# Kernel tuning notes

Hardware: AMD Instinct MI355X
Metric: run time of the kernel (lower is better)

Reference implementation:

```python
import jax, jax.numpy as jnp
import numpy as np

ND, NZ = 8192, 4096        # drug / disease node counts
IN, HID = 256, 128         # in_dim / hidden_dim
MID = (IN + HID) // 2      # projector mid width = 192
P = 4                      # metapaths per node type
M = P + 1                  # +1 raw-feature channel
DEG = 32                   # avg degree of each metapath adjacency


def _spmm_agg(feat, att, src, dst, n):
    # feat (n,IN); att (M,n,1) (only first P rows used, like the torch zip); src,dst (P,E)
    def one(a, s, d):
        deg = jax.ops.segment_sum(jnp.ones(s.shape, jnp.float32), s, num_segments=n)
        inv = 1.0 / jnp.maximum(deg, 1.0)          # L1 row-normalized adjacency values
        x = a * feat                               # node-feature attention gating (n,IN)
        return jax.ops.segment_sum(inv[s][:, None] * x[d], s, num_segments=n)
    agg = jax.vmap(one)(att[:P], src, dst)         # (P,n,IN)
    return jnp.concatenate([feat[None], agg], axis=0)   # (M,n,IN): raw feat + metapath aggs


def _projector(x, W1, b1, W2, b2, W3, b3):
    # per-metapath 3-layer MLP (dropout is eval-mode identity)
    h = jax.nn.relu(jnp.einsum('mni,mio->mno', x, W1) + b1[:, None, :])
    h = jax.nn.relu(jnp.einsum('mni,mio->mno', h, W2) + b2[:, None, :])
    return jnp.einsum('mni,mio->mno', h, W3) + b3[:, None, :]   # (M,n,HID)


def _metapath_attn(proj, Wq, bq, Wk, bk, beta):
    # per-node attention over the M metapath channels; V is computed but unused in the original
    p = jnp.transpose(proj, (1, 0, 2))             # (n,M,HID)
    q = p @ Wq + bq
    k = p @ Wk + bk
    attn = jax.nn.softmax(jnp.einsum('nmh,nkh->nmk', q, k), axis=-1)
    out = beta * jnp.einsum('nmk,nkh->nmh', attn, p) + p        # (n,M,HID)
    return out.reshape(M, p.shape[0], HID)         # faithful torch .view (NOT a transpose)


def reference(feat_drug, feat_disease, att_drug, att_disease,
              drug_src, drug_dst, disease_src, disease_dst,
              dW1, db1, dW2, db2, dW3, db3,
              zW1, zb1, zW2, zb2, zW3, zb3,
              Wq_d, bq_d, Wk_d, bk_d, beta_d,
              Wq_z, bq_z, Wk_z, bk_z, beta_z,
              weight_attn, Wdec, bdec):
    aggr_d = _spmm_agg(feat_drug, att_drug, drug_src, drug_dst, ND)
    aggr_z = _spmm_agg(feat_disease, att_disease, disease_src, disease_dst, NZ)
    proj_d = _projector(aggr_d, dW1, db1, dW2, db2, dW3, db3)          # (M,ND,HID)
    proj_z = _projector(aggr_z, zW1, zb1, zW2, zb2, zW3, zb3)          # (M,NZ,HID)
    out_d = _metapath_attn(proj_d, Wq_d, bq_d, Wk_d, bk_d, beta_d)     # (M,ND,HID)
    out_z = _metapath_attn(proj_z, Wq_z, bq_z, Wk_z, bk_z, beta_z)     # (M,NZ,HID)
    # Multiplex inner-product decoder
    dec_z = jnp.einsum('mzh,mhk->mzk', out_z, Wdec) + bdec[:, None, :]
    preds = jnp.einsum('mdh,mzh->mdz', out_d, dec_z)                   # (M,ND,NZ)
    w = jax.nn.softmax(weight_attn, axis=0)                            # (M,1,1)
    return jnp.sum(preds * w, axis=0)                                  # (ND,NZ)


def setup_inputs() -> dict:
    key = jax.random.key(0)
    ks = iter(jax.random.split(key, 48))
    f32 = jnp.float32
    def nrm(shape, scale=0.05):
        return jax.random.normal(next(ks), shape, f32) * scale
    inp = {}
    inp['feat_drug'] = nrm((ND, IN), 1.0)
    inp['feat_disease'] = nrm((NZ, IN), 1.0)
    inp['att_drug'] = jax.random.uniform(next(ks), (M, ND, 1), f32)
    inp['att_disease'] = jax.random.uniform(next(ks), (M, NZ, 1), f32)
    inp['drug_src'] = jax.random.randint(next(ks), (P, ND * DEG), 0, ND, jnp.int32)
    inp['drug_dst'] = jax.random.randint(next(ks), (P, ND * DEG), 0, ND, jnp.int32)
    inp['disease_src'] = jax.random.randint(next(ks), (P, NZ * DEG), 0, NZ, jnp.int32)
    inp['disease_dst'] = jax.random.randint(next(ks), (P, NZ * DEG), 0, NZ, jnp.int32)
    for t in ('d', 'z'):
        inp[t + 'W1'] = nrm((M, IN, MID));  inp[t + 'b1'] = jnp.zeros((M, MID), f32)
        inp[t + 'W2'] = nrm((M, MID, MID)); inp[t + 'b2'] = jnp.zeros((M, MID), f32)
        inp[t + 'W3'] = nrm((M, MID, HID)); inp[t + 'b3'] = jnp.zeros((M, HID), f32)
        inp['Wq_' + t] = nrm((HID, HID));   inp['bq_' + t] = jnp.zeros((HID,), f32)
        inp['Wk_' + t] = nrm((HID, HID));   inp['bk_' + t] = jnp.zeros((HID,), f32)
        inp['beta_' + t] = jnp.ones((1,), f32)
    inp['weight_attn'] = nrm((M, 1, 1), 1.0)
    inp['Wdec'] = nrm((M, HID, HID))
    inp['bdec'] = jnp.zeros((M, HID), f32)
    return inp
```

## Files before the change

kernel.cpp:

```cpp
#include <hip/hip_runtime.h>
#include <hip/hip_bf16.h>

#define ND 8192
#define NZ 4096
#define IN_DIM 256
#define HID 128
#define MIDW 192
#define NP 4
#define NCH 5
#define DEG 32
#define E_D (ND*DEG)
#define E_Z (NZ*DEG)
#define CAP 96

typedef __hip_bfloat16 bf16;
typedef __attribute__((ext_vector_type(8))) short s8v;
typedef __attribute__((ext_vector_type(4))) float f4v;

static __device__ __forceinline__ unsigned short f2bf(float x){
  bf16 b = __float2bfloat16(x);
  return *reinterpret_cast<unsigned short*>(&b);
}
static __device__ __forceinline__ uint packbf2(float a, float b){
  return (uint)f2bf(a) | ((uint)f2bf(b) << 16);
}
static __device__ __forceinline__ float bfl(uint w){ return __uint_as_float(w<<16); }
static __device__ __forceinline__ float bfh(uint w){ return __uint_as_float(w & 0xffff0000u); }
static __device__ __forceinline__ void gload16(const void* g, void* l){
  __builtin_amdgcn_global_load_lds(
      (const __attribute__((address_space(1))) unsigned int*)g,
      (__attribute__((address_space(3))) unsigned int*)l, 16, 0, 0);
}

static __device__ __forceinline__ void tpz(const float* __restrict__ in, bf16* __restrict__ out,
                                           int rows, int cols, long idx){
  int per = rows*cols;
  int b = (int)(idx / per);
  int rem = (int)(idx - (long)b*per);
  int r = rem / cols, c = rem - r*cols;
  out[(long)b*per + (long)c*rows + r] = __float2bfloat16(in[idx]);
}

#define B_SD 0
#define B_SZ 4096
#define B_CD 6144
#define B_CZ 8192
#define B_W1D 9216
#define B_W1Z 10176
#define B_W2D 11136
#define B_W2Z 11856
#define B_W3D 12576
#define B_W3Z 13056
#define B_WDEC 13536
#define B_G 13856
#define B_V 13984
#define B_END 13985

__global__ __launch_bounds__(256) void k_prep(
    const int* __restrict__ src_d, const int* __restrict__ dst_d,
    const int* __restrict__ src_z, const int* __restrict__ dst_z,
    int* __restrict__ cur_d, int* __restrict__ cur_z,
    int* __restrict__ edl_d, int* __restrict__ edl_z,
    const float* feat_d, const float* feat_z, bf16* featb_d, bf16* featb_z,
    const float* dW1, const float* dW2, const float* dW3,
    const float* zW1, const float* zW2, const float* zW3,
    bf16* w1t_d, bf16* w2t_d, bf16* w3t_d, bf16* w1t_z, bf16* w2t_z, bf16* w3t_z,
    const float* Wdec, bf16* wdect,
    const float* Wq_d, const float* Wk_d, const float* Wq_z, const float* Wk_z,
    bf16* Gtb,
    const float* bq_d, const float* bq_z, float* v2v,
    const float* wattn, float* wsm)
{
  int b = blockIdx.x, t = threadIdx.x;
  if (b < B_SZ){
    long i = (long)b*256 + t;
    int m = (int)(i >> 18);
    int s = src_d[i];
    int pos = atomicAdd(&cur_d[(m<<13) + s], 1);
    if (pos < CAP) edl_d[((long)((m<<13) + s))*CAP + pos] = dst_d[i];
  } else if (b < B_CD){
    long j = (long)(b - B_SZ)*256 + t;
    int m = (int)(j >> 17);
    int s = src_z[j];
    int pos = atomicAdd(&cur_z[(m<<12) + s], 1);
    if (pos < CAP) edl_z[((long)((m<<12) + s))*CAP + pos] = dst_z[j];
  } else if (b < B_CZ){
    long i4 = (long)(b - B_CD)*256 + t;
    float4 v = ((const float4*)feat_d)[i4];
    ushort4 o; o.x=f2bf(v.x); o.y=f2bf(v.y); o.z=f2bf(v.z); o.w=f2bf(v.w);
    ((ushort4*)featb_d)[i4] = o;
  } else if (b < B_W1D){
    long i4 = (long)(b - B_CZ)*256 + t;
    float4 v = ((const float4*)feat_z)[i4];
    ushort4 o; o.x=f2bf(v.x); o.y=f2bf(v.y); o.z=f2bf(v.z); o.w=f2bf(v.w);
    ((ushort4*)featb_z)[i4] = o;
  } else if (b < B_W1Z){ tpz(dW1, w1t_d, IN_DIM, MIDW, (long)(b-B_W1D)*256 + t); }
  else if (b < B_W2D){ tpz(zW1, w1t_z, IN_DIM, MIDW, (long)(b-B_W1Z)*256 + t); }
  else if (b < B_W2Z){ tpz(dW2, w2t_d, MIDW, MIDW, (long)(b-B_W2D)*256 + t); }
  else if (b < B_W3D){ tpz(zW2, w2t_z, MIDW, MIDW, (long)(b-B_W2Z)*256 + t); }
  else if (b < B_W3Z){ tpz(dW3, w3t_d, MIDW, HID, (long)(b-B_W3D)*256 + t); }
  else if (b < B_WDEC){ tpz(zW3, w3t_z, MIDW, HID, (long)(b-B_W3Z)*256 + t); }
  else if (b < B_G){ tpz(Wdec, wdect, HID, HID, (long)(b-B_WDEC)*256 + t); }
  else if (b < B_V){
    int cc = (b - B_G)*2 + (t>>7);
    int hp = t & 127;
    const float* Wq = cc < 128 ? Wq_d : Wq_z;
    const float* Wk = cc < 128 ? Wk_d : Wk_z;
    int c = cc & 127;
    float s = 0.f;
    for (int j=0;j<HID;j++) s += Wq[hp*HID+j]*Wk[c*HID+j];
    Gtb[(cc < 128 ? 0 : HID*HID) + c*HID + hp] = __float2bfloat16(s);
  } else {
    if (t < 128){
      float s = 0.f;
      for (int j=0;j<HID;j++) s += Wk_d[t*HID+j]*bq_d[j];
      v2v[t] = s;
    } else {
      int tt = t-128;
      float s = 0.f;
      for (int j=0;j<HID;j++) s += Wk_z[tt*HID+j]*bq_z[j];
      v2v[128+tt] = s;
    }
    if (t == 0){
      float mx = wattn[0];
      for (int i=1;i<NCH;i++) mx = fmaxf(mx, wattn[i]);
      float e[NCH], s=0.f;
      for (int i=0;i<NCH;i++){ e[i]=expf(wattn[i]-mx); s+=e[i]; }
      for (int i=0;i<NCH;i++) wsm[i]=e[i]/s;
    }
  }
}

__global__ __launch_bounds__(256) void k_stage1(
    const bf16* __restrict__ featb_d, const bf16* __restrict__ featb_z,
    const bf16* __restrict__ w1t_d, const bf16* __restrict__ w1t_z,
    const float* __restrict__ db1, const float* __restrict__ zb1,
    const float* __restrict__ att_d, const float* __restrict__ att_z,
    bf16* __restrict__ h1_d, bf16* __restrict__ h1_z,
    bf16* __restrict__ Y_d, bf16* __restrict__ Y_z)
{
  int z = blockIdx.z, typ = z/5, c = z - 5*(z/5);
  int n = typ ? NZ : ND;
  long row0 = (long)blockIdx.x*128;
  if (row0 >= n) return;
  int col0 = blockIdx.y*64;
  __shared__ short As[128*40];
  __shared__ short Bs[64*40];
  int t = threadIdx.x, lane = t&63, wv = t>>6;
  int l15 = lane&15, kof = (lane>>4)*8;
  const short* Ag = (const short*)(typ ? featb_z : featb_d);
  const short* Bg = (const short*)(typ ? w1t_z : w1t_d) + (long)c*MIDW*IN_DIM;
  f4v acc[2][4] = {};
  for (int kk=0; kk<IN_DIM; kk+=32){
    __syncthreads();
    #pragma unroll
    for (int j=0;j<2;j++){
      int c2 = t + j*256;
      int row = c2>>2, sub = c2&3;
      *(s8v*)(&As[row*40 + sub*8]) = *(const s8v*)(Ag + (row0+row)*IN_DIM + kk + sub*8);
    }
    { int row = t>>2, sub = t&3;
      *(s8v*)(&Bs[row*40 + sub*8]) = *(const s8v*)(Bg + (long)(col0+row)*IN_DIM + kk + sub*8); }
    __syncthreads();
    s8v af[2], bfr[4];
    #pragma unroll
    for (int i2=0;i2<2;i2++) af[i2] = *(const s8v*)(&As[(wv*32 + i2*16 + l15)*40 + kof]);
    #pragma unroll
    for (int j2=0;j2<4;j2++) bfr[j2] = *(const s8v*)(&Bs[(j2*16 + l15)*40 + kof]);
    #pragma unroll
    for (int i2=0;i2<2;i2++)
      #pragma unroll
      for (int j2=0;j2<4;j2++)
        acc[i2][j2] = __builtin_amdgcn_mfma_f32_16x16x32_bf16(af[i2], bfr[j2], acc[i2][j2],0,0,0);
  }
  if (c == 0){
    const float* bb = typ ? zb1 : db1;
    bf16* outp = typ ? h1_z : h1_d;
    #pragma unroll
    for (int i2=0;i2<2;i2++)
      #pragma unroll
      for (int j2=0;j2<4;j2++){
        int col = col0 + j2*16 + l15;
        float bv = bb[col];
        #pragma unroll
        for (int r=0;r<4;r++){
          long row = row0 + wv*32 + i2*16 + (lane>>4)*4 + r;
          outp[row*MIDW + col] = __float2bfloat16(fmaxf(acc[i2][j2][r] + bv, 0.f));
        }
      }
  } else {
    const float* rs = (typ ? att_z : att_d) + (long)(c-1)*n;
    bf16* outp = (typ ? Y_z : Y_d) + (long)(c-1)*n*MIDW;
    #pragma unroll
    for (int i2=0;i2<2;i2++)
      #pragma unroll
      for (int j2=0;j2<4;j2++){
        int col = col0 + j2*16 + l15;
        #pragma unroll
        for (int r=0;r<4;r++){
          long row = row0 + wv*32 + i2*16 + (lane>>4)*4 + r;
          outp[row*MIDW + col] = __float2bfloat16(acc[i2][j2][r] * rs[row]);
        }
      }
  }
}

__global__ __launch_bounds__(256) void k_agg2(
    const int* __restrict__ edl_d, const int* __restrict__ cur_d, const float* __restrict__ bias_d,
    const bf16* __restrict__ Y_d, bf16* __restrict__ h1_d,
    const int* __restrict__ edl_z, const int* __restrict__ cur_z, const float* __restrict__ bias_z,
    const bf16* __restrict__ Y_z, bf16* __restrict__ h1_z)
{
  int wid = (blockIdx.x*256 + threadIdx.x) >> 6;
  int lane = threadIdx.x & 63;
  const int *edl, *cur; const float* bias; const uint* Yb; bf16* h1; int n, m;
  if (wid < NP*ND){
    m = wid >> 13; int s0 = wid & (ND-1);
    edl = edl_d; cur = cur_d; bias = bias_d; h1 = h1_d; n = ND;
    Yb = (const uint*)Y_d + (long)m*ND*96;
    wid = s0;
  } else {
    int w2 = wid - NP*ND;
    m = w2 >> 12; int s0 = w2 & (NZ-1);
    edl = edl_z; cur = cur_z; bias = bias_z; h1 = h1_z; n = NZ;
    Yb = (const uint*)Y_z + (long)m*NZ*96;
    wid = s0;
  }
  int s = wid;
  int cnt0 = cur[(long)m*n + s];
  int cnt = cnt0 < CAP ? cnt0 : CAP;
  const int* lp = edl + ((long)m*n + s)*CAP;
  bool hi2 = lane < 32;
  float a0=0.f,a1=0.f,a2=0.f,a3=0.f;
  for (int base=0; base<cnt; base+=64){
    int rem = cnt - base;
    int idx = (lane < rem) ? lane : (rem-1);
    int e = lp[base + idx];
    int lim = rem < 64 ? rem : 64;
    int j = 0;
    for (; j+1<lim; j+=2){
      int d0 = __shfl(e, j), d1 = __shfl(e, j+1);
      const uint* r0 = Yb + (long)d0*96;
      const uint* r1 = Yb + (long)d1*96;
      uint w0 = r0[lane], w1 = r1[lane];
      uint v0 = hi2 ? r0[64+lane] : 0u;
      uint v1 = hi2 ? r1[64+lane] : 0u;
      a0 += bfl(w0)+bfl(w1); a1 += bfh(w0)+bfh(w1);
      a2 += bfl(v0)+bfl(v1); a3 += bfh(v0)+bfh(v1);
    }
    if (j < lim){
      int d0 = __shfl(e, j);
      const uint* r0 = Yb + (long)d0*96;
      uint w0 = r0[lane];
      uint v0 = hi2 ? r0[64+lane] : 0u;
      a0 += bfl(w0); a1 += bfh(w0);
      a2 += bfl(v0); a3 += bfh(v0);
    }
  }
  float inv = 1.0f / fmaxf((float)cnt0, 1.0f);
  const float* bb = bias + (m+1)*MIDW;
  float2 b0 = *(const float2*)(bb + 2*lane);
  uint* hrow = (uint*)((short*)h1 + ((long)(m+1)*n + s)*MIDW);
  hrow[lane] = packbf2(fmaxf(a0*inv + b0.x, 0.f), fmaxf(a1*inv + b0.y, 0.f));
  if (hi2){
    float2 b1v = *(const float2*)(bb + 128 + 2*lane);
    hrow[64+lane] = packbf2(fmaxf(a2*inv + b1v.x, 0.f), fmaxf(a3*inv + b1v.y, 0.f));
  }
}

struct GemmP {
  const bf16* A; const bf16* BT; const float* bias; bf16* out;
  const float* scale; const float* rowsc;
  long rs_moff, a_moff, out_rstride, out_moff;
  int K, N, nrows, relu;
};

__global__ __launch_bounds__(256) void k_gemm(GemmP P0, GemmP P1, int zsplit)
{
  const GemmP& p = ((int)blockIdx.z < zsplit) ? P0 : P1;
  int m = ((int)blockIdx.z < zsplit) ? blockIdx.z : blockIdx.z - zsplit;
  long row0 = (long)blockIdx.x*128;
  if (row0 >= p.nrows) return;
  int col0 = blockIdx.y*64;
  if (col0 >= p.N) return;
  __shared__ short As[128*40];
  __shared__ short Bs[64*40];
  int t = threadIdx.x;
  const short* Ag = (const short*)p.A + m*p.a_moff;
  const short* Bg = (const short*)p.BT + (long)m*p.N*p.K;
  int lane = t&63, wv = t>>6;
  int l15 = lane&15, kof = (lane>>4)*8;
  int K = p.K;
  f4v acc[2][4] = {};
  for (int kk=0; kk<K; kk+=32){
    __syncthreads();
    #pragma unroll
    for (int j=0;j<2;j++){
      int c = t + j*256;
      int row = c>>2, sub = c&3;
      *(s8v*)(&As[row*40 + sub*8]) = *(const s8v*)(Ag + (row0+row)*K + kk + sub*8);
    }
    { int row = t>>2, sub = t&3;
      *(s8v*)(&Bs[row*40 + sub*8]) = *(const s8v*)(Bg + (long)(col0+row)*K + kk + sub*8); }
    __syncthreads();
    s8v af[2], bfr[4];
    #pragma unroll
    for (int i2=0;i2<2;i2++) af[i2] = *(const s8v*)(&As[(wv*32 + i2*16 + l15)*40 + kof]);
    #pragma unroll
    for (int j2=0;j2<4;j2++) bfr[j2] = *(const s8v*)(&Bs[(j2*16 + l15)*40 + kof]);
    #pragma unroll
    for (int i2=0;i2<2;i2++)
      #pragma unroll
      for (int j2=0;j2<4;j2++)
        acc[i2][j2] = __builtin_amdgcn_mfma_f32_16x16x32_bf16(af[i2], bfr[j2], acc[i2][j2],0,0,0);
  }
  float sc = p.scale ? p.scale[m] : 1.0f;
  #pragma unroll
  for (int i2=0;i2<2;i2++){
    #pragma unroll
    for (int j2=0;j2<4;j2++){
      int col = col0 + j2*16 + l15;
      float bv = p.bias ? p.bias[m*p.N + col] : 0.f;
      #pragma unroll
      for (int r=0;r<4;r++){
        long row = row0 + wv*32 + i2*16 + (lane>>4)*4 + r;
        float v = acc[i2][j2][r] + bv;
        if (p.relu) v = fmaxf(v, 0.f);
        v *= sc;
        if (p.rowsc) v *= p.rowsc[m*p.rs_moff + row];
        p.out[m*p.out_moff + row*p.out_rstride + col] = __float2bfloat16(v);
      }
    }
  }
}

struct MlpP { const bf16* h1; const bf16* w2t; const float* b2;
              const bf16* w3t; const float* b3; bf16* pout; bf16* pgout;
              const bf16* gt; int n; };

__global__ __launch_bounds__(256) void k_mlp23(MlpP P0, MlpP P1, int zsplit)
{
  const MlpP& p = ((int)blockIdx.z < zsplit) ? P0 : P1;
  int m = ((int)blockIdx.z < zsplit) ? blockIdx.z : blockIdx.z - zsplit;
  int row0 = blockIdx.x*128;
  if (row0 >= p.n) return;
  __shared__ short h2s[128*200];
  __shared__ short As[128*40];
  __shared__ short Bs[192*40];
  int t = threadIdx.x, lane = t&63, wv = t>>6;
  int l15 = lane&15, hi = lane>>4, kof = hi*8;
  const short* Ag = (const short*)p.h1 + ((long)m*p.n + row0)*MIDW;
  const short* Bg = (const short*)p.w2t + (long)m*MIDW*MIDW;
  f4v accA[2][12] = {};
  for (int kk=0; kk<MIDW; kk+=32){
    __syncthreads();
    #pragma unroll
    for (int j=0;j<2;j++){
      int c = t + j*256;
      int row = c>>2, sub = c&3;
      *(s8v*)(&As[row*40 + sub*8]) = *(const s8v*)(Ag + (long)row*MIDW + kk + sub*8);
    }
    #pragma unroll
    for (int j=0;j<3;j++){
      int c = t + j*256;
      int row = c>>2, sub = c&3;
      *(s8v*)(&Bs[row*40 + sub*8]) = *(const s8v*)(Bg + (long)row*MIDW + kk + sub*8);
    }
    __syncthreads();
    s8v af[2], bfr[12];
    #pragma unroll
    for (int i2=0;i2<2;i2++) af[i2] = *(const s8v*)(&As[(wv*32 + i2*16 + l15)*40 + kof]);
    #pragma unroll
    for (int j2=0;j2<12;j2++) bfr[j2] = *(const s8v*)(&Bs[(j2*16 + l15)*40 + kof]);
    #pragma unroll
    for (int i2=0;i2<2;i2++)
      #pragma unroll
      for (int j2=0;j2<12;j2++)
        accA[i2][j2] = __builtin_amdgcn_mfma_f32_16x16x32_bf16(af[i2], bfr[j2], accA[i2][j2],0,0,0);
  }
  float b2l[12];
  #pragma unroll
  for (int j2=0;j2<12;j2++) b2l[j2] = p.b2[m*MIDW + j2*16 + l15];
  #pragma unroll
  for (int i2=0;i2<2;i2++)
    #pragma unroll
    for (int j2=0;j2<12;j2++)
      #pragma unroll
      for (int r=0;r<4;r++){
        int rl = wv*32 + i2*16 + hi*4 + r;
        h2s[rl*200 + j2*16 + l15] = (short)f2bf(fmaxf(accA[i2][j2][r] + b2l[j2], 0.f));
      }
  const short* Cg = (const short*)p.w3t + (long)m*HID*MIDW;
  f4v accB[2][8] = {};
  for (int kk=0; kk<MIDW; kk+=32){
    __syncthreads();
    #pragma unroll
    for (int j=0;j<2;j++){
      int c = t + j*256;
      int row = c>>2, sub = c&3;
      *(s8v*)(&Bs[row*40 + sub*8]) = *(const s8v*)(Cg + (long)row*MIDW + kk + sub*8);
    }
    __syncthreads();
    s8v af[2], bfr[8];
    #pragma unroll
    for (int i2=0;i2<2;i2++) af[i2] = *(const s8v*)(&h2s[(wv*32 + i2*16 + l15)*200 + kk + kof]);
    #pragma unroll
    for (int j2=0;j2<8;j2++) bfr[j2] = *(const s8v*)(&Bs[(j2*16 + l15)*40 + kof]);
    #pragma unroll
    for (int i2=0;i2<2;i2++)
      #pragma unroll
      for (int j2=0;j2<8;j2++)
        accB[i2][j2] = __builtin_amdgcn_mfma_f32_16x16x32_bf16(af[i2], bfr[j2], accB[i2][j2],0,0,0);
  }
  __syncthreads();
  #pragma unroll
  for (int j2=0;j2<8;j2++){
    float b3v = p.b3[m*HID + j2*16 + l15];
    #pragma unroll
    for (int i2=0;i2<2;i2++)
      #pragma unroll
      for (int r=0;r<4;r++){
        int rl = wv*32 + i2*16 + hi*4 + r;
        unsigned short hv = f2bf(accB[i2][j2][r] + b3v);
        p.pout[((long)(row0+rl))*(NCH*HID) + m*HID + j2*16 + l15] = *(bf16*)&hv;
        h2s[rl*200 + j2*16 + l15] = (short)hv;
      }
  }
  const short* Gg = (const short*)p.gt;
  f4v accC[2][8] = {};
  for (int kk=0; kk<HID; kk+=32){
    __syncthreads();
    #pragma unroll
    for (int j=0;j<2;j++){
      int c = t + j*256;
      int row = c>>2, sub = c&3;
      *(s8v*)(&Bs[row*40 + sub*8]) = *(const s8v*)(Gg + (long)row*HID + kk + sub*8);
    }
    __syncthreads();
    s8v af[2], bfr[8];
    #pragma unroll
    for (int i2=0;i2<2;i2++) af[i2] = *(const s8v*)(&h2s[(wv*32 + i2*16 + l15)*200 + kk + kof]);
    #pragma unroll
    for (int j2=0;j2<8;j2++) bfr[j2] = *(const s8v*)(&Bs[(j2*16 + l15)*40 + kof]);
    #pragma unroll
    for (int i2=0;i2<2;i2++)
      #pragma unroll
      for (int j2=0;j2<8;j2++)
        accC[i2][j2] = __builtin_amdgcn_mfma_f32_16x16x32_bf16(af[i2], bfr[j2], accC[i2][j2],0,0,0);
  }
  #pragma unroll
  for (int j2=0;j2<8;j2++)
    #pragma unroll
    for (int i2=0;i2<2;i2++)
      #pragma unroll
      for (int r=0;r<4;r++){
        long row = row0 + wv*32 + i2*16 + hi*4 + r;
        p.pgout[row*(NCH*HID) + m*HID + j2*16 + l15] = __float2bfloat16(accC[i2][j2][r]);
      }
}

__global__ __launch_bounds__(64) void k_attn(
    const bf16* __restrict__ p_d, const bf16* __restrict__ pg_d, const float* __restrict__ v2v,
    const float* __restrict__ beta_d, bf16* __restrict__ o_d,
    const bf16* __restrict__ p_z, const bf16* __restrict__ pg_z,
    const float* __restrict__ beta_z, bf16* __restrict__ o_z)
{
  int node = blockIdx.x; int t = threadIdx.x;
  const bf16 *pp, *gg; bf16* outp; const float *betap, *v2p;
  if (node < ND){
    pp = p_d + (long)node*640; gg = pg_d + (long)node*640;
    outp = o_d + (long)node*640; betap = beta_d; v2p = v2v;
  } else {
    int nz = node - ND;
    pp = p_z + (long)nz*640; gg = pg_z + (long)nz*640;
    outp = o_z + (long)nz*640; betap = beta_z; v2p = v2v + 128;
  }
  __shared__ float pl[640], gl[640], v2l[128];
  __shared__ float lg[25], at[25], bv[5];
  const uint* pu = (const uint*)pp;
  const uint* gu = (const uint*)gg;
  for (int i=t; i<320; i+=64){
    uint w = pu[i];
    pl[2*i] = bfl(w); pl[2*i+1] = bfh(w);
    uint g = gu[i];
    gl[2*i] = bfl(g); gl[2*i+1] = bfh(g);
  }
  v2l[t] = v2p[t]; v2l[64+t] = v2p[64+t];
  __syncthreads();
  if (t < 60){
    int pr = t>>1, sub = t&1, h0 = sub*64;
    float s = 0.f;
    if (pr < 25){
      int mi = pr/5, ki = pr - 5*(pr/5);
      for (int h=h0; h<h0+64; h++) s += gl[mi*HID+h]*pl[ki*HID+h];
      s += __shfl_xor(s, 1);
      if (!sub) lg[pr] = s;
    } else {
      int k = pr - 25;
      for (int h=h0; h<h0+64; h++) s += pl[k*HID+h]*v2l[h];
      s += __shfl_xor(s, 1);
      if (!sub) bv[k] = s;
    }
  }
  __syncthreads();
  if (t < 5){
    float l0[5];
    for (int j=0;j<5;j++) l0[j] = lg[t*5+j] + bv[j];
    float mx = l0[0];
    for (int j=1;j<5;j++) mx = fmaxf(mx, l0[j]);
    float e[5], su=0.f;
    for (int j=0;j<5;j++){ e[j] = expf(l0[j]-mx); su += e[j]; }
    for (int j=0;j<5;j++) at[t*5+j] = e[j]/su;
  }
  __syncthreads();
  float bt = betap[0];
  for (int i=t; i<320; i+=64){
    int mm = i>>6, h = (i&63)*2;
    float s0=0.f, s1=0.f;
    #pragma unroll
    for (int k2=0;k2<5;k2++){
      s0 += at[mm*5+k2]*pl[k2*HID+h];
      s1 += at[mm*5+k2]*pl[k2*HID+h+1];
    }
    ((uint*)outp)[i] = packbf2(pl[2*i] + bt*s0, pl[2*i+1] + bt*s1);
  }
}

__global__ __launch_bounds__(256) void k_gemm_final(
    const bf16* __restrict__ Aout, const bf16* __restrict__ Bb, float* __restrict__ out)
{
  __shared__ short As[128*64];
  __shared__ short Bs[128*64];
  int t = threadIdx.x;
  int lane = t&63, wv=t>>6, wr=wv>>1, wc=wv&1;
  int row0 = blockIdx.x*128, col0 = blockIdx.y*128;
  const short* Ag = (const short*)Aout;
  const short* Bg = (const short*)Bb;
  int l15 = lane&15, hi = lane>>4;
  int srow = t>>3;
  int sseg = (t&7) ^ (srow&7);
  f4v acc[4][4] = {};
  for (int kk=0; kk<NCH*HID; kk+=64){
    int mch = kk>>7, h0 = kk&127;
    __syncthreads();
    #pragma unroll
    for (int j=0;j<4;j++){
      int row = j*32 + srow;
      gload16(Ag + ((long)mch*ND + row0+row)*HID + h0 + sseg*8,
              (char*)As + ((j*256 + t)<<4));
      gload16(Bg + (long)(col0+row)*(NCH*HID) + kk + sseg*8,
              (char*)Bs + ((j*256 + t)<<4));
    }
    asm volatile("s_waitcnt vmcnt(0)" ::: "memory");
    __syncthreads();
    #pragma unroll
    for (int sl=0; sl<2; sl++){
      s8v af[4], bg[4];
      #pragma unroll
      for (int i=0;i<4;i++){
        int ra = wr*64 + i*16 + l15;
        af[i] = *(const s8v*)(&As[ra*64 + (((sl*4+hi) ^ (ra&7))*8)]);
        int rb = wc*64 + i*16 + l15;
        bg[i] = *(const s8v*)(&Bs[rb*64 + (((sl*4+hi) ^ (rb&7))*8)]);
      }
      #pragma unroll
      for (int mi=0;mi<4;mi++)
        #pragma unroll
        for (int ni=0;ni<4;ni++)
          acc[mi][ni] = __builtin_amdgcn_mfma_f32_16x16x32_bf16(af[mi], bg[ni], acc[mi][ni],0,0,0);
    }
  }
  #pragma unroll
  for (int mi=0;mi<4;mi++){
    #pragma unroll
    for (int ni=0;ni<4;ni++){
      int col = col0 + wc*64 + ni*16 + l15;
      #pragma unroll
      for (int r=0;r<4;r++){
        int row = row0 + wr*64 + mi*16 + hi*4 + r;
        out[(long)row*NZ + col] = acc[mi][ni][r];
      }
    }
  }
}

extern "C" void kernel_launch(void* const* d_in, const int* in_sizes, int n_in,
                              void* d_out, int out_size, void* d_ws, size_t ws_size,
                              hipStream_t stream)
{
  (void)in_sizes; (void)n_in; (void)out_size;
  const float* feat_d = (const float*)d_in[0];
  const float* feat_z = (const float*)d_in[1];
  const float* att_d  = (const float*)d_in[2];
  const float* att_z  = (const float*)d_in[3];
  const int* src_d = (const int*)d_in[4];
  const int* dst_d = (const int*)d_in[5];
  const int* src_z = (const int*)d_in[6];
  const int* dst_z = (const int*)d_in[7];
  const float* dW1=(const float*)d_in[8];  const float* db1=(const float*)d_in[9];
  const float* dW2=(const float*)d_in[10]; const float* db2=(const float*)d_in[11];
  const float* dW3=(const float*)d_in[12]; const float* db3=(const float*)d_in[13];
  const float* Wq_d=(const float*)d_in[14]; const float* bq_d=(const float*)d_in[15];
  const float* Wk_d=(const float*)d_in[16]; const float* bk_d=(const float*)d_in[17];
  const float* beta_d=(const float*)d_in[18];
  const float* zW1=(const float*)d_in[19]; const float* zb1=(const float*)d_in[20];
  const float* zW2=(const float*)d_in[21]; const float* zb2=(const float*)d_in[22];
  const float* zW3=(const float*)d_in[23]; const float* zb3=(const float*)d_in[24];
  const float* Wq_z=(const float*)d_in[25]; const float* bq_z=(const float*)d_in[26];
  const float* Wk_z=(const float*)d_in[27]; const float* bk_z=(const float*)d_in[28];
  const float* beta_z=(const float*)d_in[29];
  const float* wattn=(const float*)d_in[30];
  const float* Wdec=(const float*)d_in[31]; const float* bdec=(const float*)d_in[32];
  (void)bk_d; (void)bk_z;

  char* ws = (char*)d_ws;
  size_t o = 0;
  auto alloc = [&](size_t bytes)->char*{
    size_t r = (o + 255) & ~(size_t)255;
    o = r + bytes;
    return ws + r;
  };
  bf16* featb_d = (bf16*)alloc((size_t)ND*IN_DIM*2);
  bf16* featb_z = (bf16*)alloc((size_t)NZ*IN_DIM*2);
  bf16* Y_d = (bf16*)alloc((size_t)NP*ND*MIDW*2);
  bf16* Y_z = (bf16*)alloc((size_t)NP*NZ*MIDW*2);
  bf16* h1_d = (bf16*)alloc((size_t)NCH*ND*MIDW*2);
  bf16* h1_z = (bf16*)alloc((size_t)NCH*NZ*MIDW*2);
  bf16* pbuf_d = (bf16*)alloc((size_t)ND*NCH*HID*2);
  int* edl_d = (int*)alloc((size_t)NP*ND*CAP*4);
  int* edl_z = (int*)alloc((size_t)NP*NZ*CAP*4);
  int* cur = (int*)alloc((size_t)(NP*ND + NP*NZ)*4);
  int* cur_d = cur;
  int* cur_z = cur + NP*ND;
  bf16* w1t_d = (bf16*)alloc((size_t)NCH*MIDW*IN_DIM*2);
  bf16* w2t_d = (bf16*)alloc((size_t)NCH*MIDW*MIDW*2);
  bf16* w3t_d = (bf16*)alloc((size_t)NCH*HID*MIDW*2);
  bf16* w1t_z = (bf16*)alloc((size_t)NCH*MIDW*IN_DIM*2);
  bf16* w2t_z = (bf16*)alloc((size_t)NCH*MIDW*MIDW*2);
  bf16* w3t_z = (bf16*)alloc((size_t)NCH*HID*MIDW*2);
  bf16* Gtb = (bf16*)alloc((size_t)2*HID*HID*2);
  bf16* wdect = (bf16*)alloc((size_t)NCH*HID*HID*2);
  float* v2v = (float*)alloc((size_t)256*4);
  float* wsm = (float*)alloc((size_t)NCH*4);
  bf16* out_d = h1_d;
  bf16* out_z = h1_z;
  bf16* pg_z  = Y_d;
  bf16* Bbig  = Y_z;
  bf16* pg_d  = (bf16*)edl_d;
  bf16* pbuf_z = (bf16*)edl_z;
  if (ws_size < o) return;

  hipMemsetAsync(cur, 0, (size_t)(NP*ND + NP*NZ)*4, stream);
  k_prep<<<B_END, 256, 0, stream>>>(src_d, dst_d, src_z, dst_z, cur_d, cur_z, edl_d, edl_z,
      feat_d, feat_z, featb_d, featb_z,
      dW1, dW2, dW3, zW1, zW2, zW3,
      w1t_d, w2t_d, w3t_d, w1t_z, w2t_z, w3t_z,
      Wdec, wdect, Wq_d, Wk_d, Wq_z, Wk_z, Gtb,
      bq_d, bq_z, v2v, wattn, wsm);
  k_stage1<<<dim3(64, 3, 10), 256, 0, stream>>>(featb_d, featb_z, w1t_d, w1t_z,
      db1, zb1, att_d, att_z, h1_d, h1_z, Y_d, Y_z);
  k_agg2<<<(NP*ND + NP*NZ)/4, 256, 0, stream>>>(edl_d, cur_d, db1, Y_d, h1_d,
                                                edl_z, cur_z, zb1, Y_z, h1_z);
  {
    MlpP pd = {h1_d, w2t_d, db2, w3t_d, db3, pbuf_d, pg_d, Gtb, ND};
    MlpP pz = {h1_z, w2t_z, zb2, w3t_z, zb3, pbuf_z, pg_z, Gtb + HID*HID, NZ};
    k_mlp23<<<dim3(64, 1, 10), 256, 0, stream>>>(pd, pz, 5);
  }
  k_attn<<<ND + NZ, 64, 0, stream>>>(pbuf_d, pg_d, v2v, beta_d, out_d,
                                     pbuf_z, pg_z, beta_z, out_z);
  {
    GemmP pz = {out_z, wdect, bdec, Bbig, wsm, nullptr, 0, (long)NZ*HID, (long)NCH*HID, HID, HID, HID, NZ, 0};
    k_gemm<<<dim3(32, 2, 5), 256, 0, stream>>>(pz, pz, 5);
  }
  k_gemm_final<<<dim3(64, 32), 256, 0, stream>>>(out_d, Bbig, (float*)d_out);
}
```

Measured before the change: 291.1 us.

## Move edge bucketing into stage-1 GEMM kernel and store neighbor lists as ushort

Edge bucketing (atomic counters plus neighbor-list writes) moves out of the prep kernel and into the front of the stage-1 GEMM kernel. Each of the 1920 blocks handles a slice of edges before its GEMM tile, so the scatter can overlap with matmul work from other blocks. Neighbor lists are stored as 16-bit indices, which halves their memory traffic in both the scatter and the aggregation gather. Workspace aliasing is reshuffled to fit the smaller buffers. Blocks that exit early for disease rows still do their edge share, and the extra atomics may delay the GEMM part of each block.

```diff
diff --git a/kernel.cpp b/kernel.cpp
--- a/kernel.cpp
+++ b/kernel.cpp
@@ -12,6 +12,8 @@
 #define E_D (ND*DEG)
 #define E_Z (NZ*DEG)
 #define CAP 96
+#define NEDGE (NP*E_D + NP*E_Z)
+#define EPB 820
 
 typedef __hip_bfloat16 bf16;
 typedef __attribute__((ext_vector_type(8))) short s8v;
@@ -41,26 +43,19 @@
   out[(long)b*per + (long)c*rows + r] = __float2bfloat16(in[idx]);
 }
 
-#define B_SD 0
-#define B_SZ 4096
-#define B_CD 6144
-#define B_CZ 8192
-#define B_W1D 9216
-#define B_W1Z 10176
-#define B_W2D 11136
-#define B_W2Z 11856
-#define B_W3D 12576
-#define B_W3Z 13056
-#define B_WDEC 13536
-#define B_G 13856
-#define B_V 13984
-#define B_END 13985
+#define B_CZ 2048
+#define B_W1D 3072
+#define B_W1Z 4032
+#define B_W2D 4992
+#define B_W2Z 5712
+#define B_W3D 6432
+#define B_W3Z 6912
+#define B_WDEC 7392
+#define B_G 7712
+#define B_V 7840
+#define B_END 7841
 
 __global__ __launch_bounds__(256) void k_prep(
-    const int* __restrict__ src_d, const int* __restrict__ dst_d,
-    const int* __restrict__ src_z, const int* __restrict__ dst_z,
-    int* __restrict__ cur_d, int* __restrict__ cur_z,
-    int* __restrict__ edl_d, int* __restrict__ edl_z,
     const float* feat_d, const float* feat_z, bf16* featb_d, bf16* featb_z,
     const float* dW1, const float* dW2, const float* dW3,
     const float* zW1, const float* zW2, const float* zW3,
@@ -72,20 +67,8 @@
     const float* wattn, float* wsm)
 {
   int b = blockIdx.x, t = threadIdx.x;
-  if (b < B_SZ){
-    long i = (long)b*256 + t;
-    int m = (int)(i >> 18);
-    int s = src_d[i];
-    int pos = atomicAdd(&cur_d[(m<<13) + s], 1);
-    if (pos < CAP) edl_d[((long)((m<<13) + s))*CAP + pos] = dst_d[i];
-  } else if (b < B_CD){
-    long j = (long)(b - B_SZ)*256 + t;
-    int m = (int)(j >> 17);
-    int s = src_z[j];
-    int pos = atomicAdd(&cur_z[(m<<12) + s], 1);
-    if (pos < CAP) edl_z[((long)((m<<12) + s))*CAP + pos] = dst_z[j];
-  } else if (b < B_CZ){
-    long i4 = (long)(b - B_CD)*256 + t;
+  if (b < B_CZ){
+    long i4 = (long)b*256 + t;
     float4 v = ((const float4*)feat_d)[i4];
     ushort4 o; o.x=f2bf(v.x); o.y=f2bf(v.y); o.z=f2bf(v.z); o.w=f2bf(v.w);
     ((ushort4*)featb_d)[i4] = o;
@@ -132,6 +115,10 @@
 }
 
 __global__ __launch_bounds__(256) void k_stage1(
+    const int* __restrict__ src_d, const int* __restrict__ dst_d,
+    const int* __restrict__ src_z, const int* __restrict__ dst_z,
+    int* __restrict__ cur_d, int* __restrict__ cur_z,
+    ushort* __restrict__ edl_d, ushort* __restrict__ edl_z,
     const bf16* __restrict__ featb_d, const bf16* __restrict__ featb_z,
     const bf16* __restrict__ w1t_d, const bf16* __restrict__ w1t_z,
     const float* __restrict__ db1, const float* __restrict__ zb1,
@@ -139,6 +126,24 @@
     bf16* __restrict__ h1_d, bf16* __restrict__ h1_z,
     bf16* __restrict__ Y_d, bf16* __restrict__ Y_z)
 {
+  int t = threadIdx.x;
+  {
+    int bid = blockIdx.x + 64*(blockIdx.y + 3*blockIdx.z);
+    int e0 = bid*EPB;
+    int e1 = e0 + EPB < NEDGE ? e0 + EPB : NEDGE;
+    for (int e = e0 + t; e < e1; e += 256){
+      if (e < NP*E_D){
+        int m = e>>18, s = src_d[e];
+        int pos = atomicAdd(&cur_d[(m<<13)+s], 1);
+        if (pos < CAP) edl_d[((long)((m<<13)+s))*CAP + pos] = (ushort)dst_d[e];
+      } else {
+        int j = e - NP*E_D;
+        int m = j>>17, s = src_z[j];
+        int pos = atomicAdd(&cur_z[(m<<12)+s], 1);
+        if (pos < CAP) edl_z[((long)((m<<12)+s))*CAP + pos] = (ushort)dst_z[j];
+      }
+    }
+  }
   int z = blockIdx.z, typ = z/5, c = z - 5*(z/5);
   int n = typ ? NZ : ND;
   long row0 = (long)blockIdx.x*128;
@@ -146,7 +151,7 @@
   int col0 = blockIdx.y*64;
   __shared__ short As[128*40];
   __shared__ short Bs[64*40];
-  int t = threadIdx.x, lane = t&63, wv = t>>6;
+  int lane = t&63, wv = t>>6;
   int l15 = lane&15, kof = (lane>>4)*8;
   const short* Ag = (const short*)(typ ? featb_z : featb_d);
   const short* Bg = (const short*)(typ ? w1t_z : w1t_d) + (long)c*MIDW*IN_DIM;
@@ -206,14 +211,14 @@
 }
 
 __global__ __launch_bounds__(256) void k_agg2(
-    const int* __restrict__ edl_d, const int* __restrict__ cur_d, const float* __restrict__ bias_d,
+    const ushort* __restrict__ edl_d, const int* __restrict__ cur_d, const float* __restrict__ bias_d,
     const bf16* __restrict__ Y_d, bf16* __restrict__ h1_d,
-    const int* __restrict__ edl_z, const int* __restrict__ cur_z, const float* __restrict__ bias_z,
+    const ushort* __restrict__ edl_z, const int* __restrict__ cur_z, const float* __restrict__ bias_z,
     const bf16* __restrict__ Y_z, bf16* __restrict__ h1_z)
 {
   int wid = (blockIdx.x*256 + threadIdx.x) >> 6;
   int lane = threadIdx.x & 63;
-  const int *edl, *cur; const float* bias; const uint* Yb; bf16* h1; int n, m;
+  const ushort* edl; const int* cur; const float* bias; const uint* Yb; bf16* h1; int n, m;
   if (wid < NP*ND){
     m = wid >> 13; int s0 = wid & (ND-1);
     edl = edl_d; cur = cur_d; bias = bias_d; h1 = h1_d; n = ND;
@@ -229,7 +234,7 @@
   int s = wid;
   int cnt0 = cur[(long)m*n + s];
   int cnt = cnt0 < CAP ? cnt0 : CAP;
-  const int* lp = edl + ((long)m*n + s)*CAP;
+  const ushort* lp = edl + ((long)m*n + s)*CAP;
   bool hi2 = lane < 32;
   float a0=0.f,a1=0.f,a2=0.f,a3=0.f;
   for (int base=0; base<cnt; base+=64){
@@ -627,8 +632,9 @@
   bf16* h1_d = (bf16*)alloc((size_t)NCH*ND*MIDW*2);
   bf16* h1_z = (bf16*)alloc((size_t)NCH*NZ*MIDW*2);
   bf16* pbuf_d = (bf16*)alloc((size_t)ND*NCH*HID*2);
-  int* edl_d = (int*)alloc((size_t)NP*ND*CAP*4);
-  int* edl_z = (int*)alloc((size_t)NP*NZ*CAP*4);
+  bf16* pbuf_z = (bf16*)alloc((size_t)NZ*NCH*HID*2);
+  ushort* edl_d = (ushort*)alloc((size_t)NP*ND*CAP*2);
+  ushort* edl_z = (ushort*)alloc((size_t)NP*NZ*CAP*2);
   int* cur = (int*)alloc((size_t)(NP*ND + NP*NZ)*4);
   int* cur_d = cur;
   int* cur_z = cur + NP*ND;
@@ -644,20 +650,20 @@
   float* wsm = (float*)alloc((size_t)NCH*4);
   bf16* out_d = h1_d;
   bf16* out_z = h1_z;
-  bf16* pg_z  = Y_d;
-  bf16* Bbig  = Y_z;
-  bf16* pg_d  = (bf16*)edl_d;
-  bf16* pbuf_z = (bf16*)edl_z;
+  bf16* pg_d = featb_d;
+  bf16* pg_z = (bf16*)edl_d;
+  bf16* Bbig = pbuf_z;
   if (ws_size < o) return;
 
   hipMemsetAsync(cur, 0, (size_t)(NP*ND + NP*NZ)*4, stream);
-  k_prep<<<B_END, 256, 0, stream>>>(src_d, dst_d, src_z, dst_z, cur_d, cur_z, edl_d, edl_z,
-      feat_d, feat_z, featb_d, featb_z,
+  k_prep<<<B_END, 256, 0, stream>>>(feat_d, feat_z, featb_d, featb_z,
       dW1, dW2, dW3, zW1, zW2, zW3,
       w1t_d, w2t_d, w3t_d, w1t_z, w2t_z, w3t_z,
       Wdec, wdect, Wq_d, Wk_d, Wq_z, Wk_z, Gtb,
       bq_d, bq_z, v2v, wattn, wsm);
-  k_stage1<<<dim3(64, 3, 10), 256, 0, stream>>>(featb_d, featb_z, w1t_d, w1t_z,
+  k_stage1<<<dim3(64, 3, 10), 256, 0, stream>>>(src_d, dst_d, src_z, dst_z,
+      cur_d, cur_z, edl_d, edl_z,
+      featb_d, featb_z, w1t_d, w1t_z,
       db1, zb1, att_d, att_z, h1_d, h1_z, Y_d, Y_z);
   k_agg2<<<(NP*ND + NP*NZ)/4, 256, 0, stream>>>(edl_d, cur_d, db1, Y_d, h1_d,
                                                 edl_z, cur_z, zb1, Y_z, h1_z);
```

After: 312.4 us. +7.3%, slower.

## Replace fixed-capacity edge buckets with compact CSR built by count, scan, scatter

Applied to the files above, without the earlier changes.

Edge grouping changes from fixed 96-slot per-node buckets of int32 destinations to an exact CSR layout. The new path counts degrees with atomics in the prep kernel, prefix-sums them in a new scan kernel, and scatters 16-bit destination indices in a new scatter kernel. The aggregation kernel then reads compact offsets and indices, which cuts the sparse-write footprint and removes the CAP truncation. In exchange it adds two launches, a second atomic pass over the edges and a serial per-metapath scan, and it re-aliases several scratch buffers.

```diff
diff --git a/kernel.cpp b/kernel.cpp
--- a/kernel.cpp
+++ b/kernel.cpp
@@ -11,7 +11,7 @@
 #define DEG 32
 #define E_D (ND*DEG)
 #define E_Z (NZ*DEG)
-#define CAP 96
+#define NEDGE (NP*E_D + NP*E_Z)
 
 typedef __hip_bfloat16 bf16;
 typedef __attribute__((ext_vector_type(8))) short s8v;
@@ -41,26 +41,23 @@
   out[(long)b*per + (long)c*rows + r] = __float2bfloat16(in[idx]);
 }
 
-#define B_SD 0
-#define B_SZ 4096
-#define B_CD 6144
-#define B_CZ 8192
-#define B_W1D 9216
-#define B_W1Z 10176
-#define B_W2D 11136
-#define B_W2Z 11856
-#define B_W3D 12576
-#define B_W3Z 13056
-#define B_WDEC 13536
-#define B_G 13856
-#define B_V 13984
-#define B_END 13985
+#define B_CTD 4096
+#define B_CTZ (B_CTD+2048)
+#define B_CVD (B_CTZ+2048)
+#define B_CVZ (B_CVD+1024)
+#define B_W1D (B_CVZ+960)
+#define B_W1Z (B_W1D+960)
+#define B_W2D (B_W1Z+720)
+#define B_W2Z (B_W2D+720)
+#define B_W3D (B_W2Z+480)
+#define B_W3Z (B_W3D+480)
+#define B_WDEC (B_W3Z+320)
+#define B_G (B_WDEC+128)
+#define B_END (B_G+1)
 
 __global__ __launch_bounds__(256) void k_prep(
-    const int* __restrict__ src_d, const int* __restrict__ dst_d,
-    const int* __restrict__ src_z, const int* __restrict__ dst_z,
-    int* __restrict__ cur_d, int* __restrict__ cur_z,
-    int* __restrict__ edl_d, int* __restrict__ edl_z,
+    const int* __restrict__ src_d, const int* __restrict__ src_z,
+    int* __restrict__ deg_d, int* __restrict__ deg_z,
     const float* feat_d, const float* feat_z, bf16* featb_d, bf16* featb_z,
     const float* dW1, const float* dW2, const float* dW3,
     const float* zW1, const float* zW2, const float* zW3,
@@ -72,37 +69,33 @@
     const float* wattn, float* wsm)
 {
   int b = blockIdx.x, t = threadIdx.x;
-  if (b < B_SZ){
+  if (b < B_CTD){
     long i = (long)b*256 + t;
     int m = (int)(i >> 18);
-    int s = src_d[i];
-    int pos = atomicAdd(&cur_d[(m<<13) + s], 1);
-    if (pos < CAP) edl_d[((long)((m<<13) + s))*CAP + pos] = dst_d[i];
-  } else if (b < B_CD){
-    long j = (long)(b - B_SZ)*256 + t;
+    atomicAdd(&deg_d[(m<<13) + src_d[i]], 1);
+  } else if (b < B_CTZ){
+    long j = (long)(b - B_CTD)*256 + t;
     int m = (int)(j >> 17);
-    int s = src_z[j];
-    int pos = atomicAdd(&cur_z[(m<<12) + s], 1);
-    if (pos < CAP) edl_z[((long)((m<<12) + s))*CAP + pos] = dst_z[j];
-  } else if (b < B_CZ){
-    long i4 = (long)(b - B_CD)*256 + t;
+    atomicAdd(&deg_z[(m<<12) + src_z[j]], 1);
+  } else if (b < B_CVD){
+    long i4 = (long)(b - B_CTZ)*256 + t;
     float4 v = ((const float4*)feat_d)[i4];
     ushort4 o; o.x=f2bf(v.x); o.y=f2bf(v.y); o.z=f2bf(v.z); o.w=f2bf(v.w);
     ((ushort4*)featb_d)[i4] = o;
-  } else if (b < B_W1D){
-    long i4 = (long)(b - B_CZ)*256 + t;
+  } else if (b < B_CVZ){
+    long i4 = (long)(b - B_CVD)*256 + t;
     float4 v = ((const float4*)feat_z)[i4];
     ushort4 o; o.x=f2bf(v.x); o.y=f2bf(v.y); o.z=f2bf(v.z); o.w=f2bf(v.w);
     ((ushort4*)featb_z)[i4] = o;
-  } else if (b < B_W1Z){ tpz(dW1, w1t_d, IN_DIM, MIDW, (long)(b-B_W1D)*256 + t); }
-  else if (b < B_W2D){ tpz(zW1, w1t_z, IN_DIM, MIDW, (long)(b-B_W1Z)*256 + t); }
-  else if (b < B_W2Z){ tpz(dW2, w2t_d, MIDW, MIDW, (long)(b-B_W2D)*256 + t); }
-  else if (b < B_W3D){ tpz(zW2, w2t_z, MIDW, MIDW, (long)(b-B_W2Z)*256 + t); }
-  else if (b < B_W3Z){ tpz(dW3, w3t_d, MIDW, HID, (long)(b-B_W3D)*256 + t); }
-  else if (b < B_WDEC){ tpz(zW3, w3t_z, MIDW, HID, (long)(b-B_W3Z)*256 + t); }
-  else if (b < B_G){ tpz(Wdec, wdect, HID, HID, (long)(b-B_WDEC)*256 + t); }
-  else if (b < B_V){
-    int cc = (b - B_G)*2 + (t>>7);
+  } else if (b < B_W1D){ tpz(dW1, w1t_d, IN_DIM, MIDW, (long)(b-B_CVZ)*256 + t); }
+  else if (b < B_W1Z){ tpz(zW1, w1t_z, IN_DIM, MIDW, (long)(b-B_W1D)*256 + t); }
+  else if (b < B_W2D){ tpz(dW2, w2t_d, MIDW, MIDW, (long)(b-B_W1Z)*256 + t); }
+  else if (b < B_W2Z){ tpz(zW2, w2t_z, MIDW, MIDW, (long)(b-B_W2D)*256 + t); }
+  else if (b < B_W3D){ tpz(dW3, w3t_d, MIDW, HID, (long)(b-B_W2Z)*256 + t); }
+  else if (b < B_W3Z){ tpz(zW3, w3t_z, MIDW, HID, (long)(b-B_W3D)*256 + t); }
+  else if (b < B_WDEC){ tpz(Wdec, wdect, HID, HID, (long)(b-B_W3Z)*256 + t); }
+  else if (b < B_G){
+    int cc = (b - B_WDEC)*2 + (t>>7);
     int hp = t & 127;
     const float* Wq = cc < 128 ? Wq_d : Wq_z;
     const float* Wk = cc < 128 ? Wk_d : Wk_z;
@@ -128,6 +121,57 @@
       for (int i=0;i<NCH;i++){ e[i]=expf(wattn[i]-mx); s+=e[i]; }
       for (int i=0;i<NCH;i++) wsm[i]=e[i]/s;
     }
+  }
+}
+
+__global__ __launch_bounds__(256) void k_scan(const int* __restrict__ deg_d, int* __restrict__ off_d,
+                                              const int* __restrict__ deg_z, int* __restrict__ off_z){
+  int b = blockIdx.x;
+  const int* d; int* o; int n;
+  if (b < NP){ d = deg_d + (long)b*ND; o = off_d + (long)b*(ND+1); n = ND; }
+  else { int m = b-NP; d = deg_z + (long)m*NZ; o = off_z + (long)m*(NZ+1); n = NZ; }
+  int t = threadIdx.x, lane = t&63, wv = t>>6;
+  __shared__ int wsum[4];
+  __shared__ int carry;
+  if (t==0) carry = 0;
+  __syncthreads();
+  for (int base=0; base<n; base+=256){
+    int v = d[base+t];
+    int x = v;
+    #pragma unroll
+    for (int s=1; s<64; s<<=1){
+      int u = __shfl_up(x, s, 64);
+      if (lane >= s) x += u;
+    }
+    if (lane==63) wsum[wv] = x;
+    __syncthreads();
+    int wo = 0;
+    for (int w=0; w<wv; w++) wo += wsum[w];
+    int c = carry;
+    o[base+t] = c + wo + x - v;
+    __syncthreads();
+    if (t==255) carry = c + wo + x;
+  }
+  __syncthreads();
+  if (t==0) o[n] = carry;
+}
+
+__global__ void k_scat(const int* __restrict__ src_d, const int* __restrict__ dst_d,
+                       const int* __restrict__ off_d, int* __restrict__ cur_d, ushort* __restrict__ csr_d,
+                       const int* __restrict__ src_z, const int* __restrict__ dst_z,
+                       const int* __restrict__ off_z, int* __restrict__ cur_z, ushort* __restrict__ csr_z){
+  long i = (long)blockIdx.x*blockDim.x + threadIdx.x;
+  if (i < (long)NP*E_D){
+    int m = (int)(i >> 18);
+    int s = src_d[i];
+    int pos = atomicAdd(&cur_d[(m<<13) + s], 1);
+    csr_d[(long)m*E_D + off_d[(long)m*(ND+1) + s] + pos] = (ushort)dst_d[i];
+  } else {
+    long j = i - (long)NP*E_D;
+    int m = (int)(j >> 17);
+    int s = src_z[j];
+    int pos = atomicAdd(&cur_z[(m<<12) + s], 1);
+    csr_z[(long)m*E_Z + off_z[(long)m*(NZ+1) + s] + pos] = (ushort)dst_z[j];
   }
 }
 
@@ -206,30 +250,32 @@
 }
 
 __global__ __launch_bounds__(256) void k_agg2(
-    const int* __restrict__ edl_d, const int* __restrict__ cur_d, const float* __restrict__ bias_d,
+    const ushort* __restrict__ csr_d, const int* __restrict__ off_d, const float* __restrict__ bias_d,
     const bf16* __restrict__ Y_d, bf16* __restrict__ h1_d,
-    const int* __restrict__ edl_z, const int* __restrict__ cur_z, const float* __restrict__ bias_z,
+    const ushort* __restrict__ csr_z, const int* __restrict__ off_z, const float* __restrict__ bias_z,
     const bf16* __restrict__ Y_z, bf16* __restrict__ h1_z)
 {
   int wid = (blockIdx.x*256 + threadIdx.x) >> 6;
   int lane = threadIdx.x & 63;
-  const int *edl, *cur; const float* bias; const uint* Yb; bf16* h1; int n, m;
+  const ushort* csr; const int* off; const float* bias; const uint* Yb; bf16* h1; int n, m; long ebase;
   if (wid < NP*ND){
     m = wid >> 13; int s0 = wid & (ND-1);
-    edl = edl_d; cur = cur_d; bias = bias_d; h1 = h1_d; n = ND;
+    csr = csr_d; off = off_d + (long)m*(ND+1); bias = bias_d; h1 = h1_d; n = ND;
     Yb = (const uint*)Y_d + (long)m*ND*96;
+    ebase = (long)m*E_D;
     wid = s0;
   } else {
     int w2 = wid - NP*ND;
     m = w2 >> 12; int s0 = w2 & (NZ-1);
-    edl = edl_z; cur = cur_z; bias = bias_z; h1 = h1_z; n = NZ;
+    csr = csr_z; off = off_z + (long)m*(NZ+1); bias = bias_z; h1 = h1_z; n = NZ;
     Yb = (const uint*)Y_z + (long)m*NZ*96;
+    ebase = (long)m*E_Z;
     wid = s0;
   }
   int s = wid;
-  int cnt0 = cur[(long)m*n + s];
-  int cnt = cnt0 < CAP ? cnt0 : CAP;
-  const int* lp = edl + ((long)m*n + s)*CAP;
+  int o0 = off[s], o1 = off[s+1];
+  int cnt = o1 - o0;
+  const ushort* lp = csr + ebase + o0;
   bool hi2 = lane < 32;
   float a0=0.f,a1=0.f,a2=0.f,a3=0.f;
   for (int base=0; base<cnt; base+=64){
@@ -257,7 +303,7 @@
       a2 += bfl(v0); a3 += bfh(v0);
     }
   }
-  float inv = 1.0f / fmaxf((float)cnt0, 1.0f);
+  float inv = 1.0f / fmaxf((float)cnt, 1.0f);
   const float* bb = bias + (m+1)*MIDW;
   float2 b0 = *(const float2*)(bb + 2*lane);
   uint* hrow = (uint*)((short*)h1 + ((long)(m+1)*n + s)*MIDW);
@@ -627,11 +673,17 @@
   bf16* h1_d = (bf16*)alloc((size_t)NCH*ND*MIDW*2);
   bf16* h1_z = (bf16*)alloc((size_t)NCH*NZ*MIDW*2);
   bf16* pbuf_d = (bf16*)alloc((size_t)ND*NCH*HID*2);
-  int* edl_d = (int*)alloc((size_t)NP*ND*CAP*4);
-  int* edl_z = (int*)alloc((size_t)NP*NZ*CAP*4);
-  int* cur = (int*)alloc((size_t)(NP*ND + NP*NZ)*4);
-  int* cur_d = cur;
-  int* cur_z = cur + NP*ND;
+  bf16* pbuf_z = (bf16*)alloc((size_t)NZ*NCH*HID*2);
+  bf16* pg_z = (bf16*)alloc((size_t)NZ*NCH*HID*2);
+  ushort* csr_d = (ushort*)alloc((size_t)NP*E_D*2);
+  ushort* csr_z = (ushort*)alloc((size_t)NP*E_Z*2);
+  int* degcur = (int*)alloc((size_t)2*(NP*ND + NP*NZ)*4);
+  int* deg_d = degcur;
+  int* deg_z = deg_d + NP*ND;
+  int* cur_d = deg_z + NP*NZ;
+  int* cur_z = cur_d + NP*ND;
+  int* off_d = (int*)alloc((size_t)NP*(ND+1)*4);
+  int* off_z = (int*)alloc((size_t)NP*(NZ+1)*4);
   bf16* w1t_d = (bf16*)alloc((size_t)NCH*MIDW*IN_DIM*2);
   bf16* w2t_d = (bf16*)alloc((size_t)NCH*MIDW*MIDW*2);
   bf16* w3t_d = (bf16*)alloc((size_t)NCH*HID*MIDW*2);
@@ -644,23 +696,24 @@
   float* wsm = (float*)alloc((size_t)NCH*4);
   bf16* out_d = h1_d;
   bf16* out_z = h1_z;
-  bf16* pg_z  = Y_d;
-  bf16* Bbig  = Y_z;
-  bf16* pg_d  = (bf16*)edl_d;
-  bf16* pbuf_z = (bf16*)edl_z;
+  bf16* pg_d = featb_d;
+  bf16* Bbig = pbuf_z;
   if (ws_size < o) return;
 
-  hipMemsetAsync(cur, 0, (size_t)(NP*ND + NP*NZ)*4, stream);
-  k_prep<<<B_END, 256, 0, stream>>>(src_d, dst_d, src_z, dst_z, cur_d, cur_z, edl_d, edl_z,
+  hipMemsetAsync(degcur, 0, (size_t)2*(NP*ND + NP*NZ)*4, stream);
+  k_prep<<<B_END, 256, 0, stream>>>(src_d, src_z, deg_d, deg_z,
       feat_d, feat_z, featb_d, featb_z,
       dW1, dW2, dW3, zW1, zW2, zW3,
       w1t_d, w2t_d, w3t_d, w1t_z, w2t_z, w3t_z,
       Wdec, wdect, Wq_d, Wk_d, Wq_z, Wk_z, Gtb,
       bq_d, bq_z, v2v, wattn, wsm);
+  k_scan<<<2*NP, 256, 0, stream>>>(deg_d, off_d, deg_z, off_z);
+  k_scat<<<NEDGE/256, 256, 0, stream>>>(src_d, dst_d, off_d, cur_d, csr_d,
+                                        src_z, dst_z, off_z, cur_z, csr_z);
   k_stage1<<<dim3(64, 3, 10), 256, 0, stream>>>(featb_d, featb_z, w1t_d, w1t_z,
       db1, zb1, att_d, att_z, h1_d, h1_z, Y_d, Y_z);
-  k_agg2<<<(NP*ND + NP*NZ)/4, 256, 0, stream>>>(edl_d, cur_d, db1, Y_d, h1_d,
-                                                edl_z, cur_z, zb1, Y_z, h1_z);
+  k_agg2<<<(NP*ND + NP*NZ)/4, 256, 0, stream>>>(csr_d, off_d, db1, Y_d, h1_d,
+                                                csr_z, off_z, zb1, Y_z, h1_z);
   {
     MlpP pd = {h1_d, w2t_d, db2, w3t_d, db3, pbuf_d, pg_d, Gtb, ND};
     MlpP pz = {h1_z, w2t_z, zb2, w3t_z, zb3, pbuf_z, pg_z, Gtb + HID*HID, NZ};
```

New measurement: 374.8 us. 1.29x slower.
